# Performance work log

Measured on AMD Instinct MI355X. Metric: run time of the kernel, lower is better.

## Reference

```python
import jax, jax.numpy as jnp
import numpy as np

C = 256      # hidden_dim
H = 8        # num_head
D = 6        # depth
NQ = 100     # num_queries
B = 4        # view pairs
FEAT_HW = [64, 32, 16, 8]


def setup_inputs() -> dict:
    key = jax.random.key(0)
    ws = C ** -0.5  # weight init scale (xavier-like)
    inp = {}
    i = 0
    def nk():
        nonlocal i
        i += 1
        return jax.random.fold_in(key, i)
    for v in (1, 2):
        for l, hw in enumerate(FEAT_HW, 1):
            inp[f"feat{v}_{l}"] = jax.random.normal(nk(), (B, C, hw, hw), jnp.float32)
    inp["query_embed"] = jax.random.uniform(nk(), (NQ, C), jnp.float32)
    inp["ca_ng"] = jnp.ones((D, C), jnp.float32)
    inp["ca_nb"] = jnp.zeros((D, C), jnp.float32)
    inp["ca_wq"] = jax.random.normal(nk(), (D, C, C), jnp.float32) * ws
    inp["ca_wk"] = jax.random.normal(nk(), (D, C, C), jnp.float32) * ws
    inp["ca_wv"] = jax.random.normal(nk(), (D, C, C), jnp.float32) * ws
    inp["ca_wp"] = jax.random.normal(nk(), (D, C, C), jnp.float32) * ws
    inp["ca_bp"] = jnp.zeros((D, C), jnp.float32)
    inp["sa_wqkv"] = jax.random.normal(nk(), (D, C, 3 * C), jnp.float32) * ws
    inp["sa_wp"] = jax.random.normal(nk(), (D, C, C), jnp.float32) * ws
    inp["sa_bp"] = jnp.zeros((D, C), jnp.float32)
    return inp


def _ln(x, g, b):
    m = jnp.mean(x, axis=-1, keepdims=True)
    v = jnp.mean((x - m) ** 2, axis=-1, keepdims=True)
    return (x - m) * jax.lax.rsqrt(v + 1e-5) * g + b


def _mha(q, k, v):
    # q: [B,Nq,C], k,v: [B,Nk,C] -> [B,Nq,C]
    b, nq, _ = q.shape
    nk = k.shape[1]
    hd = C // H
    q = q.reshape(b, nq, H, hd)
    k = k.reshape(b, nk, H, hd)
    v = v.reshape(b, nk, H, hd)
    a = jnp.einsum('bqhd,bkhd->bhqk', q, k) * (hd ** -0.5)
    a = jax.nn.softmax(a, axis=-1)
    o = jnp.einsum('bhqk,bkhd->bqhd', a, v)
    return o.reshape(b, nq, C)


def reference(feat1_1, feat1_2, feat1_3, feat1_4,
              feat2_1, feat2_2, feat2_3, feat2_4,
              query_embed, ca_ng, ca_nb, ca_wq, ca_wk, ca_wv, ca_wp, ca_bp,
              sa_wqkv, sa_wp, sa_bp):
    def tok(f):  # [B,C,h,w] -> [B,h*w,C]
        return f.reshape(f.shape[0], C, -1).transpose(0, 2, 1)
    feats1 = [tok(f) for f in (feat1_1, feat1_2, feat1_3, feat1_4)]
    feats2 = [tok(f) for f in (feat2_1, feat2_2, feat2_3, feat2_4)]
    outs = []
    for f1, f2 in zip(feats1, feats2):
        q = jnp.broadcast_to(query_embed, (B, NQ, C))
        for d in range(D):
            # self attention (output replaces queries, as in the source)
            qkv = q @ sa_wqkv[d]
            qq, kk, vv = jnp.split(qkv, 3, axis=-1)
            q = _mha(qq, kk, vv) @ sa_wp[d] + sa_bp[d]
            # cross attention into each view's feature tokens
            def cross(xq, xkv):
                qn = _ln(xq, ca_ng[d], ca_nb[d]) @ ca_wq[d]
                kn = _ln(xkv, ca_ng[d], ca_nb[d]) @ ca_wk[d]
                vn = _ln(xkv, ca_ng[d], ca_nb[d]) @ ca_wv[d]
                return _mha(qn, kn, vn) @ ca_wp[d] + ca_bp[d]
            q1 = cross(q, f1)
            q2 = cross(q, f2)
            ms = jnp.einsum('bic,bjc->bij', q1, q2)  # [B,NQ,NQ] matching score
            r1 = q1 + jnp.einsum('bij,bjd->bid', jax.nn.softmax(ms, axis=2), q2)
            r2 = q2 + jnp.einsum('bij,bid->bjd', jax.nn.softmax(ms, axis=1), q1)
            q = jax.nn.softmax(q + r1 + r2, axis=-1)
        outs.append(q)
    return jnp.stack(outs)  # [num_layers, B, NQ, C]
```

## Files before the change

### kernel.cpp

```cpp
#include <hip/hip_runtime.h>


#define DI __device__ __forceinline__
#define MFMA16(a, b, c) __builtin_amdgcn_mfma_f32_16x16x32_bf16(a, b, c, 0, 0, 0)

typedef __attribute__((ext_vector_type(8))) short bf16x8;
typedef __attribute__((ext_vector_type(8))) unsigned short u16x8;
typedef __attribute__((ext_vector_type(4))) float f32x4;

constexpr long KVV = 5570560;

constexpr long O_KH    = 0;
constexpr long O_KL    = O_KH    + 5570560;
constexpr long O_VTH   = O_KL    + 5570560;
constexpr long O_VTL   = O_VTH   + 5570560;
constexpr long O_QBUF  = O_VTL   + 5570560;
constexpr long O_QKV   = O_QBUF  + 409600;
constexpr long O_QSA   = O_QKV   + 1228800;
constexpr long O_QHAT  = O_QSA   + 409600;
constexpr long O_QN    = O_QHAT  + 409600;
constexpr long O_SAO   = O_QN    + 409600;
constexpr long O_OCA   = O_SAO   + 409600;
constexpr long O_Q12   = O_OCA   + 819200;
constexpr long O_QH    = O_Q12   + 819200;
constexpr long O_QL    = O_QH    + 208896;
constexpr long O_WTH   = O_QL    + 208896;
constexpr long O_WTL   = O_WTH   + 393216;
constexpr long O_WQH   = O_WTL   + 393216;
constexpr long O_WQL   = O_WQH   + 196608;
constexpr long O_BKV   = O_WQL   + 196608;
constexpr long O_BQ    = O_BKV   + 3072;
constexpr long O_PO    = O_BQ    + 1536;
constexpr long O_PM    = O_PO    + 409600;
constexpr long O_PL    = O_PM    + 16384;
constexpr long O_PO2   = O_PL    + 16384;
constexpr long O_PM2   = O_PO2   + 3145728;
constexpr long O_PL2   = O_PM2   + 98304;
constexpr long O_MS    = O_PL2   + 98304;
constexpr long O_RST   = O_MS    + 262144;
constexpr long O_STATS = O_RST   + 8192;
constexpr long O_XH    = O_STATS + 87040;
constexpr long O_XL    = O_XH    + 5570560;
constexpr long O_SQKVH = O_XL    + 5570560;
constexpr long O_SQKVL = O_SQKVH + 589824;
constexpr long O_SWPH  = O_SQKVL + 589824;
constexpr long O_SWPL  = O_SWPH  + 196608;
constexpr long O_WPH   = O_SWPL  + 196608;
constexpr long O_WPL   = O_WPH   + 196608;
constexpr long WS_FLOATS = O_WPL + 196608;

DI int sel4(int4 v, int i) { return i == 0 ? v.x : (i == 1 ? v.y : (i == 2 ? v.z : v.w)); }
DI float dot4(float4 a, float4 b) {
  float s = a.x * b.x;
  s = fmaf(a.y, b.y, s); s = fmaf(a.z, b.z, s); s = fmaf(a.w, b.w, s);
  return s;
}
DI unsigned short bf_rne(float x) {
  unsigned u = __float_as_uint(x);
  u += 0x7fffu + ((u >> 16) & 1u);
  return (unsigned short)(u >> 16);
}
DI float bf2f(unsigned short h) { return __uint_as_float(((unsigned)h) << 16); }
DI long frag_off(int nblk_base, int k, int n) {
  return ((long)(nblk_base + (n >> 4)) * 8 + (k >> 5)) * 512 +
         ((((k & 31) >> 3)) * 16 + (n & 15)) * 8 + (k & 7);
}

__global__ void fold_w2_kernel(const float* __restrict__ ng, const float* __restrict__ wk,
                               const float* __restrict__ wv, const float* __restrict__ wq,
                               unsigned short* __restrict__ WTh, unsigned short* __restrict__ WTl,
                               unsigned short* __restrict__ WQh, unsigned short* __restrict__ WQl) {
  long idx = (long)blockIdx.x * 256 + threadIdx.x;
  const long T1 = 6L * 512 * 256;
  if (idx < T1) {
    int d = idx / (512 * 256); int r = idx % (512 * 256); int n = r / 256; int k = r % 256;
    float g = ng[d * 256 + k];
    float w = (n < 256) ? wk[((long)(d * 256 + k)) * 256 + n]
                        : wv[((long)(d * 256 + k)) * 256 + (n - 256)];
    w *= g;
    unsigned short hi = bf_rne(w);
    long off = frag_off(d * 32, k, n);
    WTh[off] = hi;
    WTl[off] = bf_rne(w - bf2f(hi));
  } else {
    long j = idx - T1;
    if (j < 6L * 256 * 256) {
      int d = j / 65536; int r = j % 65536; int k = r / 256; int n = r % 256;
      float w = ng[d * 256 + k] * wq[((long)(d * 256 + k)) * 256 + n];
      unsigned short hi = bf_rne(w);
      long off = frag_off(d * 16, k, n);
      WQh[off] = hi;
      WQl[off] = bf_rne(w - bf2f(hi));
    }
  }
}

__global__ void split_wall_kernel(const float* __restrict__ swqkv,
                                  const float* __restrict__ swp,
                                  const float* __restrict__ wp,
                                  unsigned short* __restrict__ SQh, unsigned short* __restrict__ SQl,
                                  unsigned short* __restrict__ SPh, unsigned short* __restrict__ SPl,
                                  unsigned short* __restrict__ WPh, unsigned short* __restrict__ WPl) {
  long idx = (long)blockIdx.x * 256 + threadIdx.x;
  const long T1 = 6L * 256 * 768;
  const long T2 = T1 + 6L * 256 * 256;
  const long T3 = T2 + 6L * 256 * 256;
  if (idx < T1) {
    int d = idx / 196608; int r = idx % 196608; int k = r / 768; int n = r % 768;
    float w = swqkv[idx];
    unsigned short hi = bf_rne(w);
    long off = frag_off(d * 48, k, n);
    SQh[off] = hi;
    SQl[off] = bf_rne(w - bf2f(hi));
  } else if (idx < T2) {
    long j = idx - T1;
    int d = j / 65536; int r = j % 65536; int k = r / 256; int n = r % 256;
    float w = swp[j];
    unsigned short hi = bf_rne(w);
    long off = frag_off(d * 16, k, n);
    SPh[off] = hi;
    SPl[off] = bf_rne(w - bf2f(hi));
  } else if (idx < T3) {
    long j = idx - T2;
    int d = j / 65536; int r = j % 65536; int k = r / 256; int n = r % 256;
    float w = wp[j];
    unsigned short hi = bf_rne(w);
    long off = frag_off(d * 16, k, n);
    WPh[off] = hi;
    WPl[off] = bf_rne(w - bf2f(hi));
  }
}

__global__ void fold_b_kernel(const float* __restrict__ nb, const float* __restrict__ wk,
                              const float* __restrict__ wv, const float* __restrict__ wq,
                              float* __restrict__ bkvo, float* __restrict__ bqo) {
  int idx = blockIdx.x * 256 + threadIdx.x;
  if (idx >= 6 * 768) return;
  int d = idx / 768, j = idx % 768;
  float s = 0.f;
  if (j < 256) {
    for (int c = 0; c < 256; ++c) s = fmaf(nb[d * 256 + c], wk[(d * 256 + c) * 256 + j], s);
    bkvo[d * 512 + j] = s;
  } else if (j < 512) {
    int n = j - 256;
    for (int c = 0; c < 256; ++c) s = fmaf(nb[d * 256 + c], wv[(d * 256 + c) * 256 + n], s);
    bkvo[d * 512 + j] = s;
  } else {
    int n = j - 512;
    for (int c = 0; c < 256; ++c) s = fmaf(nb[d * 256 + c], wq[(d * 256 + c) * 256 + n], s);
    bqo[d * 256 + n] = s;
  }
}

__global__ __launch_bounds__(256) void ln_stats_kernel(const float* __restrict__ feat,
                                                       float* __restrict__ stats,
                                                       int rowBase, int HW) {
  __shared__ float sred[4][64];
  __shared__ float qred[4][64];
  int b = blockIdx.y, t0 = blockIdx.x * 64;
  int tx = threadIdx.x & 63, ty = threadIdx.x >> 6;
  const float* fb = feat + (long)b * 256 * HW;
  float s = 0.f, q = 0.f;
  for (int k = 0; k < 64; ++k) {
    int c = ty * 64 + k;
    float v = fb[(long)c * HW + t0 + tx];
    s += v; q += v * v;
  }
  sred[ty][tx] = s; qred[ty][tx] = q;
  __syncthreads();
  if (ty == 0) {
    float ts = sred[0][tx] + sred[1][tx] + sred[2][tx] + sred[3][tx];
    float tq = qred[0][tx] + qred[1][tx] + qred[2][tx] + qred[3][tx];
    float m = ts * (1.f / 256.f);
    float var = tq * (1.f / 256.f) - m * m;
    int row = rowBase + b * HW + t0 + tx;
    stats[row * 2 + 0] = m;
    stats[row * 2 + 1] = rsqrtf(var + 1e-5f);
  }
}

__global__ __launch_bounds__(256) void ln_split_x_kernel(
    const float* __restrict__ f0, const float* __restrict__ f1,
    const float* __restrict__ f2, const float* __restrict__ f3,
    const float* __restrict__ stats, int vbase,
    unsigned short* __restrict__ Xh, unsigned short* __restrict__ Xl) {
  __shared__ unsigned short Th[64][66], Tl[64][66];
  int m0 = blockIdx.x * 64;
  const float* fp; int HW, rel;
  if (m0 < 16384)      { fp = f0; HW = 4096; rel = m0; }
  else if (m0 < 20480) { fp = f1; HW = 1024; rel = m0 - 16384; }
  else if (m0 < 21504) { fp = f2; HW = 256;  rel = m0 - 20480; }
  else                 { fp = f3; HW = 64;   rel = m0 - 21504; }
  int b = rel / HW, t0 = rel % HW;
  const float* fb = fp + (long)b * 256 * HW + t0;
  int t = threadIdx.x & 63, cg4 = threadIdx.x >> 6;
  float mean = stats[(vbase + m0 + t) * 2 + 0];
  float rstd = stats[(vbase + m0 + t) * 2 + 1];
  long mtb = (long)((vbase + m0) >> 4);
  int lmt = threadIdx.x >> 6, lane = threadIdx.x & 63;
  int fr = lane & 15, g = lane >> 4;
  for (int cgo = 0; cgo < 4; ++cgo) {
    if (cgo) __syncthreads();
#pragma unroll
    for (int i = 0; i < 16; ++i) {
      int c = cgo * 64 + cg4 * 16 + i;
      float x = (fb[(long)c * HW + t] - mean) * rstd;
      unsigned short hi = bf_rne(x);
      Th[t][cg4 * 16 + i] = hi;
      Tl[t][cg4 * 16 + i] = bf_rne(x - bf2f(hi));
    }
    __syncthreads();
#pragma unroll
    for (int sk = 0; sk < 2; ++sk) {
      u16x8 vh = *(const u16x8*)&Th[lmt * 16 + fr][sk * 32 + 8 * g];
      u16x8 vl = *(const u16x8*)&Tl[lmt * 16 + fr][sk * 32 + 8 * g];
      long dst = ((mtb + lmt) * 8 + cgo * 2 + sk) * 512 + lane * 8;
      *(u16x8*)&Xh[dst] = vh;
      *(u16x8*)&Xl[dst] = vl;
    }
  }
}

__global__ void init_q_kernel(const float* __restrict__ qe, float* __restrict__ qb) {
  int idx = blockIdx.x * 256 + threadIdx.x;
  if (idx < 1600 * 256) {
    int row = idx >> 8, c = idx & 255;
    qb[idx] = qe[(row % 100) * 256 + c];
  }
}

__global__ void split_q_kernel(const float* __restrict__ qn,
                               unsigned short* __restrict__ Qh,
                               unsigned short* __restrict__ Ql) {
  int idx = blockIdx.x * 256 + threadIdx.x;
  if (idx >= 1632 * 256) return;
  float v = (idx < 1600 * 256) ? qn[idx] * 0.17677669529663689f : 0.f;
  unsigned short hi = bf_rne(v);
  Qh[idx] = hi;
  Ql[idx] = bf_rne(v - bf2f(hi));
}

__global__ __launch_bounds__(256) void gemm_mfma_kernel(
    const float* __restrict__ A,
    const unsigned short* __restrict__ Wh, const unsigned short* __restrict__ Wl,
    const float* __restrict__ bias, float* __restrict__ C, int N) {
  __shared__ unsigned short Ah[2][8][512], Al[2][8][512];
  int n0 = blockIdx.x * 128;
  int m0 = blockIdx.y * 32;
  int tid = threadIdx.x;
  int w = tid >> 6, lane = tid & 63;
  int fr = lane & 15, g = lane >> 4;
#pragma unroll
  for (int mt = 0; mt < 2; ++mt)
#pragma unroll
    for (int kk = 0; kk < 2; ++kk) {
      int ks = 2 * w + kk;
      const float* src = &A[(long)(m0 + mt * 16 + fr) * 256 + ks * 32 + 8 * g];
      float4 f0 = *(const float4*)src;
      float4 f1 = *(const float4*)(src + 4);
      float vals[8] = {f0.x, f0.y, f0.z, f0.w, f1.x, f1.y, f1.z, f1.w};
      union { u16x8 v; unsigned short us[8]; } hh, ll;
#pragma unroll
      for (int e = 0; e < 8; ++e) {
        unsigned short hi = bf_rne(vals[e]);
        hh.us[e] = hi;
        ll.us[e] = bf_rne(vals[e] - bf2f(hi));
      }
      *(u16x8*)&Ah[mt][ks][lane * 8] = hh.v;
      *(u16x8*)&Al[mt][ks][lane * 8] = ll.v;
    }
  __syncthreads();
  f32x4 acc[2][2];
#pragma unroll
  for (int c4 = 0; c4 < 2; ++c4)
#pragma unroll
    for (int mt = 0; mt < 2; ++mt)
#pragma unroll
      for (int r = 0; r < 4; ++r) acc[c4][mt][r] = 0.f;
  for (int ks = 0; ks < 8; ++ks) {
    bf16x8 ah[2], al[2], wh[2], wl[2];
#pragma unroll
    for (int mt = 0; mt < 2; ++mt) {
      ah[mt] = *(const bf16x8*)&Ah[mt][ks][lane * 8];
      al[mt] = *(const bf16x8*)&Al[mt][ks][lane * 8];
    }
#pragma unroll
    for (int c4 = 0; c4 < 2; ++c4) {
      long wb = ((long)((n0 >> 4) + w * 2 + c4) * 8 + ks) * 512 + lane * 8;
      wh[c4] = *(const bf16x8*)&Wh[wb];
      wl[c4] = *(const bf16x8*)&Wl[wb];
    }
#pragma unroll
    for (int c4 = 0; c4 < 2; ++c4)
#pragma unroll
      for (int mt = 0; mt < 2; ++mt) {
        acc[c4][mt] = MFMA16(wh[c4], ah[mt], acc[c4][mt]);
        acc[c4][mt] = MFMA16(wh[c4], al[mt], acc[c4][mt]);
        acc[c4][mt] = MFMA16(wl[c4], ah[mt], acc[c4][mt]);
      }
  }
#pragma unroll
  for (int c4 = 0; c4 < 2; ++c4) {
    int nb = n0 + w * 32 + c4 * 16 + 4 * g;
    float4 bv = make_float4(0.f, 0.f, 0.f, 0.f);
    if (bias) bv = *(const float4*)&bias[nb];
#pragma unroll
    for (int mt = 0; mt < 2; ++mt) {
      int token = m0 + mt * 16 + fr;
      float4 o;
      o.x = acc[c4][mt][0] + bv.x;
      o.y = acc[c4][mt][1] + bv.y;
      o.z = acc[c4][mt][2] + bv.z;
      o.w = acc[c4][mt][3] + bv.w;
      *(float4*)&C[(long)token * N + nb] = o;
    }
  }
}

__global__ __launch_bounds__(256) void gemm_kv8_kernel(
    const unsigned short* __restrict__ Xh, const unsigned short* __restrict__ Xl,
    const unsigned short* __restrict__ Wh, const unsigned short* __restrict__ Wl,
    const float* __restrict__ bias,
    unsigned short* __restrict__ Kh, unsigned short* __restrict__ Kl,
    unsigned short* __restrict__ VTh, unsigned short* __restrict__ VTl) {
  __shared__ unsigned short Tls[18432];
  int nh = blockIdx.x;
  int m0 = blockIdx.y * 64;
  int v = blockIdx.z;
  int tid = threadIdx.x;
  int w = tid >> 6, lane = tid & 63;
  int fr = lane & 15, g = lane >> 4;
  long xmtb = (long)(v * 1360 + blockIdx.y * 4);
  f32x4 acc[4][4];
#pragma unroll
  for (int c4 = 0; c4 < 4; ++c4)
#pragma unroll
    for (int mt = 0; mt < 4; ++mt)
#pragma unroll
      for (int r = 0; r < 4; ++r) acc[c4][mt][r] = 0.f;
  for (int ks = 0; ks < 8; ++ks) {
    bf16x8 xh_[4], xl_[4], wh_[4], wl_[4];
#pragma unroll
    for (int mt = 0; mt < 4; ++mt) {
      long ar = ((xmtb + mt) * 8 + ks) * 512 + lane * 8;
      xh_[mt] = *(const bf16x8*)&Xh[ar];
      xl_[mt] = *(const bf16x8*)&Xl[ar];
    }
#pragma unroll
    for (int c4 = 0; c4 < 4; ++c4) {
      long br = ((long)(nh * 16 + c4 * 4 + w) * 8 + ks) * 512 + lane * 8;
      wh_[c4] = *(const bf16x8*)&Wh[br];
      wl_[c4] = *(const bf16x8*)&Wl[br];
    }
    if (nh == 0) {
#pragma unroll
      for (int c4 = 0; c4 < 4; ++c4)
#pragma unroll
        for (int mt = 0; mt < 4; ++mt) {
          acc[c4][mt] = MFMA16(wh_[c4], xh_[mt], acc[c4][mt]);
          acc[c4][mt] = MFMA16(wh_[c4], xl_[mt], acc[c4][mt]);
          acc[c4][mt] = MFMA16(wl_[c4], xh_[mt], acc[c4][mt]);
        }
    } else {
#pragma unroll
      for (int c4 = 0; c4 < 4; ++c4)
#pragma unroll
        for (int mt = 0; mt < 4; ++mt) {
          acc[c4][mt] = MFMA16(xh_[mt], wh_[c4], acc[c4][mt]);
          acc[c4][mt] = MFMA16(xl_[mt], wh_[c4], acc[c4][mt]);
          acc[c4][mt] = MFMA16(xh_[mt], wl_[c4], acc[c4][mt]);
        }
    }
  }
  long kvoff = (long)v * KVV;
  long tbb = (long)(m0 >> 5);
  if (nh == 0) {
    for (int part = 0; part < 2; ++part) {
      __syncthreads();
#pragma unroll
      for (int c4 = 0; c4 < 4; ++c4) {
        int nb = c4 * 64 + w * 16 + 4 * g;
        float4 bv4 = *(const float4*)&bias[nb];
        float bvs[4] = {bv4.x, bv4.y, bv4.z, bv4.w};
#pragma unroll
        for (int mt = 0; mt < 4; ++mt) {
          int tok = mt * 16 + fr;
          ushort4 u;
#pragma unroll
          for (int r = 0; r < 4; ++r) {
            float val = acc[c4][mt][r] + bvs[r];
            unsigned short hi = bf_rne(val);
            ((unsigned short*)&u)[r] = (part == 0) ? hi : bf_rne(val - bf2f(hi));
          }
          *(ushort4*)&Tls[tok * 264 + nb] = u;
        }
      }
      __syncthreads();
      unsigned short* dst = (part == 0) ? Kh : Kl;
#pragma unroll
      for (int i = 0; i < 8; ++i) {
        int gid = tid + 256 * i;
        int lane2 = gid & 63;
        int rest = gid >> 6;
        int t16 = rest & 1;
        int h2 = (rest >> 1) & 7;
        int tb_loc = rest >> 4;
        int fr2 = lane2 & 15, g2 = lane2 >> 4;
        int row = tb_loc * 32 + 8 * (fr2 >> 2) + (fr2 & 3) + 4 * t16;
        u16x8 val = *(const u16x8*)&Tls[row * 264 + h2 * 32 + 8 * g2];
        long off = kvoff + (((tbb + tb_loc) * 8 + h2) * 2 + t16) * 512 + lane2 * 8;
        *(u16x8*)&dst[off] = val;
      }
    }
  } else {
    for (int part = 0; part < 2; ++part) {
      __syncthreads();
#pragma unroll
      for (int c4 = 0; c4 < 4; ++c4) {
        int nv = c4 * 64 + w * 16 + fr;
        float bv = bias[256 + nv];
#pragma unroll
        for (int mt = 0; mt < 4; ++mt) {
          int tok = mt * 16 + 4 * g;
          ushort4 u;
#pragma unroll
          for (int r = 0; r < 4; ++r) {
            float val = acc[c4][mt][r] + bv;
            unsigned short hi = bf_rne(val);
            ((unsigned short*)&u)[r] = (part == 0) ? hi : bf_rne(val - bf2f(hi));
          }
          *(ushort4*)&Tls[nv * 72 + tok] = u;
        }
      }
      __syncthreads();
      unsigned short* dst = (part == 0) ? VTh : VTl;
#pragma unroll
      for (int i = 0; i < 8; ++i) {
        int gid = tid + 256 * i;
        int lane2 = gid & 63;
        int rest = gid >> 6;
        int d16 = rest & 1;
        int h2 = (rest >> 1) & 7;
        int tb_loc = rest >> 4;
        int fr2 = lane2 & 15, g2 = lane2 >> 4;
        int row = h2 * 32 + d16 * 16 + fr2;
        int col = tb_loc * 32 + 8 * g2;
        u16x8 val = *(const u16x8*)&Tls[row * 72 + col];
        long off = kvoff + (((tbb + tb_loc) * 8 + h2) * 2 + d16) * 512 + lane2 * 8;
        *(u16x8*)&dst[off] = val;
      }
    }
  }
}

__global__ __launch_bounds__(256) void row_ln_kernel(const float* __restrict__ in,
                                                     float* __restrict__ out) {
  __shared__ float s1[4], s2[4];
  long r = blockIdx.x;
  float x = in[r * 256 + threadIdx.x];
  float vs = x, vq = x * x;
  for (int o = 32; o; o >>= 1) { vs += __shfl_xor(vs, o); vq += __shfl_xor(vq, o); }
  int w = threadIdx.x >> 6;
  if ((threadIdx.x & 63) == 0) { s1[w] = vs; s2[w] = vq; }
  __syncthreads();
  float ts = s1[0] + s1[1] + s1[2] + s1[3];
  float tq = s2[0] + s2[1] + s2[2] + s2[3];
  float m = ts * (1.f / 256.f);
  float var = tq * (1.f / 256.f) - m * m;
  out[r * 256 + threadIdx.x] = (x - m) * rsqrtf(var + 1e-5f);
}

__global__ __launch_bounds__(256) void flash_kernel(const float* __restrict__ qp, int qld,
                                                    const float* __restrict__ kb,
                                                    const float* __restrict__ vb, int kvld,
                                                    int4 startv, int4 nchv, int4 nkv,
                                                    int4 koffv, int4 kstrbv,
                                                    float* __restrict__ po,
                                                    float* __restrict__ pm,
                                                    float* __restrict__ pl) {
  __shared__ float Kt[32][36];
  __shared__ float Vt[32][36];
  int bid = blockIdx.x;
  int s1 = startv.y, s2 = startv.z, s3 = startv.w;
  int l = (bid < s1) ? 0 : (bid < s2) ? 1 : (bid < s3) ? 2 : 3;
  int r = bid - sel4(startv, l);
  int nc = sel4(nchv, l);
  int b = r / (8 * nc);
  int h = (r / nc) & 7;
  int ch = r % nc;
  int Nk = sel4(nkv, l);
  int qr0 = (l * 4 + b) * 100;
  int kr0 = sel4(koffv, l) + b * sel4(kstrbv, l);
  int j0 = ch * 128;
  int jn = min(128, Nk - j0);
  int tiles = (jn + 31) >> 5;
  int tid = threadIdx.x;
  int qi = tid >> 1, half = tid & 1, ho = half * 16, jb = half * 16;
  const float SC = 0.17677669529663689f;
  float4 q8[8];
  if (qi < 100) {
    const float* qrow = qp + (long)(qr0 + qi) * qld + h * 32;
#pragma unroll
    for (int k = 0; k < 8; ++k) {
      float4 f = *(const float4*)&qrow[4 * k];
      q8[k] = make_float4(f.x * SC, f.y * SC, f.z * SC, f.w * SC);
    }
  } else {
#pragma unroll
    for (int k = 0; k < 8; ++k) q8[k] = make_float4(0.f, 0.f, 0.f, 0.f);
  }
  float m = -1e30f, lsum = 0.f;
  float o[16];
#pragma unroll
  for (int i = 0; i < 16; ++i) o[i] = 0.f;

  for (int kt = 0; kt < tiles; ++kt) {
    __syncthreads();
    {
      int rr = tid >> 3, c4 = (tid & 7) * 4;
      int jr = kt * 32 + rr;
      float4 kf = make_float4(0.f, 0.f, 0.f, 0.f), vf = kf;
      if (jr < jn) {
        long g = (long)(kr0 + j0 + jr) * kvld + h * 32 + c4;
        kf = *(const float4*)&kb[g];
        vf = *(const float4*)&vb[g];
      }
      *(float4*)&Kt[rr][c4 ^ (rr & 16)] = kf;
      *(float4*)&Vt[rr][c4] = vf;
    }
    __syncthreads();
    float sv[16];
#pragma unroll
    for (int j = 0; j < 16; ++j) {
      float s = 0.f;
#pragma unroll
      for (int k4 = 0; k4 < 8; ++k4) {
        float4 kv = *(const float4*)&Kt[jb + j][(4 * k4) ^ jb];
        s = fmaf(q8[k4].x, kv.x, s); s = fmaf(q8[k4].y, kv.y, s);
        s = fmaf(q8[k4].z, kv.z, s); s = fmaf(q8[k4].w, kv.w, s);
      }
      int jglob = j0 + kt * 32 + jb + j;
      sv[j] = (jglob < Nk) ? s : -1e30f;
    }
    float tmax = sv[0];
#pragma unroll
    for (int j = 1; j < 16; ++j) tmax = fmaxf(tmax, sv[j]);
    tmax = fmaxf(tmax, __shfl_xor(tmax, 1));
    float mnew = fmaxf(m, tmax);
    float scale = __expf(m - mnew);
    float p[16]; float psum = 0.f;
#pragma unroll
    for (int j = 0; j < 16; ++j) {
      int jglob = j0 + kt * 32 + jb + j;
      float e = (jglob < Nk) ? __expf(sv[j] - mnew) : 0.f;
      p[j] = e; psum += e;
    }
    psum += __shfl_xor(psum, 1);
    lsum = lsum * scale + psum;
    m = mnew;
#pragma unroll
    for (int i = 0; i < 16; ++i) o[i] *= scale;
    float pO[16];
#pragma unroll
    for (int j = 0; j < 16; ++j) pO[j] = __shfl_xor(p[j], 1);
    int jbO = jb ^ 16;
#pragma unroll
    for (int j = 0; j < 16; ++j) {
      float pj = p[j];
      const float* vrow = &Vt[jb + j][ho];
#pragma unroll
      for (int k = 0; k < 4; ++k) {
        float4 v4 = *(const float4*)&vrow[4 * k];
        o[4 * k + 0] = fmaf(pj, v4.x, o[4 * k + 0]);
        o[4 * k + 1] = fmaf(pj, v4.y, o[4 * k + 1]);
        o[4 * k + 2] = fmaf(pj, v4.z, o[4 * k + 2]);
        o[4 * k + 3] = fmaf(pj, v4.w, o[4 * k + 3]);
      }
    }
#pragma unroll
    for (int j = 0; j < 16; ++j) {
      float pj = pO[j];
      const float* vrow = &Vt[jbO + j][ho];
#pragma unroll
      for (int k = 0; k < 4; ++k) {
        float4 v4 = *(const float4*)&vrow[4 * k];
        o[4 * k + 0] = fmaf(pj, v4.x, o[4 * k + 0]);
        o[4 * k + 1] = fmaf(pj, v4.y, o[4 * k + 1]);
        o[4 * k + 2] = fmaf(pj, v4.z, o[4 * k + 2]);
        o[4 * k + 3] = fmaf(pj, v4.w, o[4 * k + 3]);
      }
    }
  }
  if (qi < 100) {
    float* pod = po + (long)bid * 3200 + qi * 32 + ho;
#pragma unroll
    for (int k = 0; k < 4; ++k)
      *(float4*)&pod[4 * k] = make_float4(o[4 * k], o[4 * k + 1], o[4 * k + 2], o[4 * k + 3]);
    if (half == 0) { pm[bid * 128 + qi] = m; pl[bid * 128 + qi] = lsum; }
  }
}

__global__ __launch_bounds__(256) void combine_kernel(const float* __restrict__ po,
                                                      const float* __restrict__ pm,
                                                      const float* __restrict__ pl,
                                                      int4 startv, int4 nchv,
                                                      float* __restrict__ outp, int outld) {
  int bid = blockIdx.x;
  int l = bid >> 5, rr = bid & 31, b = rr >> 3, h = rr & 7;
  int nc = sel4(nchv, l);
  int sb = sel4(startv, l) + (b * 8 + h) * nc;
  int qr0 = (l * 4 + b) * 100;
  int idx = blockIdx.y * 256 + threadIdx.x;
  if (idx >= 3200) return;
  int qi = idx >> 5, hd = idx & 31;
  float mstar = -1e30f;
  for (int c = 0; c < nc; ++c) mstar = fmaxf(mstar, pm[(sb + c) * 128 + qi]);
  float Lt = 0.f, val = 0.f;
  for (int c = 0; c < nc; ++c) {
    float w = __expf(pm[(sb + c) * 128 + qi] - mstar);
    Lt = fmaf(w, pl[(sb + c) * 128 + qi], Lt);
    val = fmaf(w, po[(long)(sb + c) * 3200 + qi * 32 + hd], val);
  }
  outp[(long)(qr0 + qi) * outld + h * 32 + hd] = val / Lt;
}

__global__ __launch_bounds__(256) void flash_ca2_kernel(
    const unsigned short* __restrict__ Qh, const unsigned short* __restrict__ Ql,
    const unsigned short* __restrict__ Kh, const unsigned short* __restrict__ Kl,
    const unsigned short* __restrict__ VTh, const unsigned short* __restrict__ VTl,
    float* __restrict__ po, float* __restrict__ pm, float* __restrict__ pl) {
  int tid = threadIdx.x;
  int uu = blockIdx.x * 4 + (tid >> 6);
  int v = uu / 1536;
  int u = uu - v * 1536;
  int lane = tid & 63;
  int fr = lane & 15, g = lane >> 4;
  int base, lognc, koff, kstr, ntile, l;
  if (u < 1024)      { base = 0;    lognc = 3; koff = 0;     kstr = 4096; ntile = 16; l = 0; }
  else if (u < 1280) { base = 1024; lognc = 1; koff = 16384; kstr = 1024; ntile = 16; l = 1; }
  else if (u < 1408) { base = 1280; lognc = 0; koff = 20480; kstr = 256;  ntile = 8;  l = 2; }
  else               { base = 1408; lognc = 0; koff = 21504; kstr = 64;   ntile = 2;  l = 3; }
  int r = u - base;
  int qg = r & 3; r >>= 2;
  int ch = r & ((1 << lognc) - 1); r >>= lognc;
  int h = r & 7, b = r >> 3;
  long kvoff = (long)v * KVV;
  long qoff = ((long)((l * 4 + b) * 100 + qg * 32)) * 256 + h * 32 + 8 * g;
  bf16x8 qh0 = *(const bf16x8*)&Qh[qoff + fr * 256];
  bf16x8 qh1 = *(const bf16x8*)&Qh[qoff + (16 + fr) * 256];
  bf16x8 ql0 = *(const bf16x8*)&Ql[qoff + fr * 256];
  bf16x8 ql1 = *(const bf16x8*)&Ql[qoff + (16 + fr) * 256];
  int tb0 = (koff + b * kstr + ch * 512) >> 5;
  f32x4 o00 = {0.f, 0.f, 0.f, 0.f}, o01 = o00, o10 = o00, o11 = o00;
  float m0r = -1e30f, m1r = -1e30f, l0r = 0.f, l1r = 0.f;

  for (int kt = 0; kt < ntile; ++kt) {
    long fb = kvoff + (((long)(tb0 + kt) * 8 + h) * 2) * 512 + lane * 8;
    bf16x8 kh0 = *(const bf16x8*)&Kh[fb];
    bf16x8 kl0 = *(const bf16x8*)&Kl[fb];
    bf16x8 kh1 = *(const bf16x8*)&Kh[fb + 512];
    bf16x8 kl1 = *(const bf16x8*)&Kl[fb + 512];
    bf16x8 vh0 = *(const bf16x8*)&VTh[fb];
    bf16x8 vl0 = *(const bf16x8*)&VTl[fb];
    bf16x8 vh1 = *(const bf16x8*)&VTh[fb + 512];
    bf16x8 vl1 = *(const bf16x8*)&VTl[fb + 512];
    f32x4 zz = {0.f, 0.f, 0.f, 0.f};
    f32x4 s00 = zz, s01 = zz, s10 = zz, s11 = zz;
    s00 = MFMA16(kh0, qh0, s00); s00 = MFMA16(kl0, qh0, s00); s00 = MFMA16(kh0, ql0, s00);
    s01 = MFMA16(kh1, qh0, s01); s01 = MFMA16(kl1, qh0, s01); s01 = MFMA16(kh1, ql0, s01);
    s10 = MFMA16(kh0, qh1, s10); s10 = MFMA16(kl0, qh1, s10); s10 = MFMA16(kh0, ql1, s10);
    s11 = MFMA16(kh1, qh1, s11); s11 = MFMA16(kl1, qh1, s11); s11 = MFMA16(kh1, ql1, s11);
    {
      float t0 = fmaxf(fmaxf(s00[0], s00[1]), fmaxf(s00[2], s00[3]));
      float t1 = fmaxf(fmaxf(s01[0], s01[1]), fmaxf(s01[2], s01[3]));
      float tm = fmaxf(t0, t1);
      tm = fmaxf(tm, __shfl_xor(tm, 16));
      tm = fmaxf(tm, __shfl_xor(tm, 32));
      float mn = fmaxf(m0r, tm);
      float sc = __expf(m0r - mn); m0r = mn;
      float p[8]; float ps = 0.f;
#pragma unroll
      for (int i = 0; i < 4; ++i) { p[i] = __expf(s00[i] - mn); ps += p[i]; }
#pragma unroll
      for (int i = 0; i < 4; ++i) { p[4 + i] = __expf(s01[i] - mn); ps += p[4 + i]; }
      l0r = l0r * sc + ps;
      union { bf16x8 v; unsigned short us[8]; } ph, plo;
#pragma unroll
      for (int e = 0; e < 8; ++e) {
        unsigned short hi = bf_rne(p[e]);
        ph.us[e] = hi;
        plo.us[e] = bf_rne(p[e] - bf2f(hi));
      }
#pragma unroll
      for (int i = 0; i < 4; ++i) { o00[i] *= sc; o01[i] *= sc; }
      o00 = MFMA16(vh0, ph.v, o00); o00 = MFMA16(vl0, ph.v, o00); o00 = MFMA16(vh0, plo.v, o00);
      o01 = MFMA16(vh1, ph.v, o01); o01 = MFMA16(vl1, ph.v, o01); o01 = MFMA16(vh1, plo.v, o01);
    }
    {
      float t0 = fmaxf(fmaxf(s10[0], s10[1]), fmaxf(s10[2], s10[3]));
      float t1 = fmaxf(fmaxf(s11[0], s11[1]), fmaxf(s11[2], s11[3]));
      float tm = fmaxf(t0, t1);
      tm = fmaxf(tm, __shfl_xor(tm, 16));
      tm = fmaxf(tm, __shfl_xor(tm, 32));
      float mn = fmaxf(m1r, tm);
      float sc = __expf(m1r - mn); m1r = mn;
      float p[8]; float ps = 0.f;
#pragma unroll
      for (int i = 0; i < 4; ++i) { p[i] = __expf(s10[i] - mn); ps += p[i]; }
#pragma unroll
      for (int i = 0; i < 4; ++i) { p[4 + i] = __expf(s11[i] - mn); ps += p[4 + i]; }
      l1r = l1r * sc + ps;
      union { bf16x8 v; unsigned short us[8]; } ph, plo;
#pragma unroll
      for (int e = 0; e < 8; ++e) {
        unsigned short hi = bf_rne(p[e]);
        ph.us[e] = hi;
        plo.us[e] = bf_rne(p[e] - bf2f(hi));
      }
#pragma unroll
      for (int i = 0; i < 4; ++i) { o10[i] *= sc; o11[i] *= sc; }
      o10 = MFMA16(vh0, ph.v, o10); o10 = MFMA16(vl0, ph.v, o10); o10 = MFMA16(vh0, plo.v, o10);
      o11 = MFMA16(vh1, ph.v, o11); o11 = MFMA16(vl1, ph.v, o11); o11 = MFMA16(vh1, plo.v, o11);
    }
  }
  l0r += __shfl_xor(l0r, 16); l0r += __shfl_xor(l0r, 32);
  l1r += __shfl_xor(l1r, 16); l1r += __shfl_xor(l1r, 32);
  long pob = (long)uu * 1024;
  *(f32x4*)&po[pob + fr * 32 + 4 * g] = o00;
  *(f32x4*)&po[pob + fr * 32 + 16 + 4 * g] = o01;
  *(f32x4*)&po[pob + (16 + fr) * 32 + 4 * g] = o10;
  *(f32x4*)&po[pob + (16 + fr) * 32 + 16 + 4 * g] = o11;
  if (g == 0) {
    pm[uu * 32 + fr] = m0r;       pl[uu * 32 + fr] = l0r;
    pm[uu * 32 + 16 + fr] = m1r;  pl[uu * 32 + 16 + fr] = l1r;
  }
}

__global__ __launch_bounds__(256) void combine2_kernel(const float* __restrict__ po,
                                                       const float* __restrict__ pm,
                                                       const float* __restrict__ pl,
                                                       float* __restrict__ oca) {
  int gu = blockIdx.x;
  int v = gu >> 9;
  int u = gu & 511;
  int l = u >> 7, ur = u & 127;
  int b = ur >> 5, h = (ur >> 2) & 7, qg = ur & 3;
  int nc, base;
  if (l == 0)      { nc = 8; base = 0; }
  else if (l == 1) { nc = 2; base = 1024; }
  else if (l == 2) { nc = 1; base = 1280; }
  else             { nc = 1; base = 1408; }
  int pu0 = v * 1536 + base + ((b * 8 + h) * nc) * 4 + qg;
  int qr0 = (l * 4 + b) * 100 + qg * 32;
  int qn = min(32, 100 - qg * 32);
  float* outp = oca + (long)v * 409600;
  for (int e = threadIdx.x; e < 1024; e += 256) {
    int qi = e >> 5, d = e & 31;
    if (qi >= qn) continue;
    float mstar = -1e30f;
    for (int c = 0; c < nc; ++c) mstar = fmaxf(mstar, pm[(pu0 + 4 * c) * 32 + qi]);
    float Lt = 0.f, val = 0.f;
    for (int c = 0; c < nc; ++c) {
      float w = __expf(pm[(pu0 + 4 * c) * 32 + qi] - mstar);
      Lt = fmaf(w, pl[(pu0 + 4 * c) * 32 + qi], Lt);
      val = fmaf(w, po[(long)(pu0 + 4 * c) * 1024 + qi * 32 + d], val);
    }
    outp[(long)(qr0 + qi) * 256 + h * 32 + d] = val / Lt;
  }
}

__global__ __launch_bounds__(256) void fuse_ms_kernel(const float* __restrict__ q1,
                                                      const float* __restrict__ q2,
                                                      float* __restrict__ ms) {
  __shared__ float a[32][132];
  __shared__ float bsh[32][132];
  int lb = blockIdx.x;
  int it = blockIdx.y >> 2, jt = blockIdx.y & 3;
  int tid = threadIdx.x;
  int ti = tid & 15, tj = tid >> 4;
  float acc[2][2] = {};
  for (int chalf = 0; chalf < 2; ++chalf) {
    __syncthreads();
#pragma unroll
    for (int k = 0; k < 4; ++k) {
      int i = tid + k * 256;
      int rr = i >> 5, c4 = (i & 31) * 4;
      int row1 = it * 32 + rr, row2 = jt * 32 + rr;
      float4 fa = make_float4(0.f, 0.f, 0.f, 0.f), fb = fa;
      if (row1 < 100) fa = *(const float4*)&q1[(long)(lb * 100 + row1) * 256 + chalf * 128 + c4];
      if (row2 < 100) fb = *(const float4*)&q2[(long)(lb * 100 + row2) * 256 + chalf * 128 + c4];
      *(float4*)&a[rr][c4] = fa;
      *(float4*)&bsh[rr][c4] = fb;
    }
    __syncthreads();
#pragma unroll
    for (int k4 = 0; k4 < 32; ++k4) {
      float4 a0 = *(const float4*)&a[2 * ti][4 * k4];
      float4 a1 = *(const float4*)&a[2 * ti + 1][4 * k4];
      float4 b0 = *(const float4*)&bsh[2 * tj][4 * k4];
      float4 b1 = *(const float4*)&bsh[2 * tj + 1][4 * k4];
      acc[0][0] += dot4(a0, b0); acc[0][1] += dot4(a0, b1);
      acc[1][0] += dot4(a1, b0); acc[1][1] += dot4(a1, b1);
    }
  }
#pragma unroll
  for (int i = 0; i < 2; ++i)
#pragma unroll
    for (int j = 0; j < 2; ++j)
      ms[(long)(lb * 128 + it * 32 + 2 * ti + i) * 128 + jt * 32 + 2 * tj + j] = acc[i][j];
}

__global__ void fuse_stats_kernel(const float* __restrict__ ms, float* __restrict__ rst) {
  int lb = blockIdx.x, tid = threadIdx.x;
  if (tid < 100) {
    const float* row = ms + (long)(lb * 128 + tid) * 128;
    float mx = row[0];
    for (int j = 1; j < 100; ++j) mx = fmaxf(mx, row[j]);
    float s = 0.f;
    for (int j = 0; j < 100; ++j) s += __expf(row[j] - mx);
    rst[(0 * 16 + lb) * 128 + tid] = mx;
    rst[(1 * 16 + lb) * 128 + tid] = s;
  } else if (tid >= 128 && tid < 228) {
    int j = tid - 128;
    const float* colp = ms + (long)lb * 128 * 128 + j;
    float mx = colp[0];
    for (int i = 1; i < 100; ++i) mx = fmaxf(mx, colp[i * 128]);
    float s = 0.f;
    for (int i = 0; i < 100; ++i) s += __expf(colp[i * 128] - mx);
    rst[(2 * 16 + lb) * 128 + j] = mx;
    rst[(3 * 16 + lb) * 128 + j] = s;
  }
}

__global__ __launch_bounds__(256) void fuse_apply_kernel(const float* __restrict__ ms,
                                                         const float* __restrict__ rst,
                                                         const float* __restrict__ q1,
                                                         const float* __restrict__ q2,
                                                         const float* __restrict__ qsa,
                                                         float* __restrict__ qout) {
  __shared__ float pr[100], pc[100];
  __shared__ float red1[4], red2[4];
  int lb = blockIdx.x, i = blockIdx.y, tid = threadIdx.x;
  long r = lb * 100 + i;
  if (tid < 100) {
    float rm = rst[(0 * 16 + lb) * 128 + i], rs = rst[(1 * 16 + lb) * 128 + i];
    pr[tid] = __expf(ms[(long)(lb * 128 + i) * 128 + tid] - rm) / rs;
  } else if (tid >= 128 && tid < 228) {
    int i2 = tid - 128;
    float cm = rst[(2 * 16 + lb) * 128 + i], cs = rst[(3 * 16 + lb) * 128 + i];
    pc[i2] = __expf(ms[(long)(lb * 128 + i2) * 128 + i] - cm) / cs;
  }
  __syncthreads();
  float acc1 = 0.f, acc2 = 0.f;
  for (int j = 0; j < 100; ++j) acc1 = fmaf(pr[j], q2[(long)(lb * 100 + j) * 256 + tid], acc1);
  for (int j = 0; j < 100; ++j) acc2 = fmaf(pc[j], q1[(long)(lb * 100 + j) * 256 + tid], acc2);
  float z = qsa[r * 256 + tid] + q1[r * 256 + tid] + acc1 + q2[r * 256 + tid] + acc2;
  float v = z;
  for (int off = 32; off; off >>= 1) v = fmaxf(v, __shfl_xor(v, off));
  int w = tid >> 6;
  if ((tid & 63) == 0) red1[w] = v;
  __syncthreads();
  float zm = fmaxf(fmaxf(red1[0], red1[1]), fmaxf(red1[2], red1[3]));
  float e = __expf(z - zm);
  float sv = e;
  for (int off = 32; off; off >>= 1) sv += __shfl_xor(sv, off);
  if ((tid & 63) == 0) red2[w] = sv;
  __syncthreads();
  float es = red2[0] + red2[1] + red2[2] + red2[3];
  qout[r * 256 + tid] = e / es;
}

extern "C" void kernel_launch(void* const* d_in, const int* in_sizes, int n_in,
                              void* d_out, int out_size, void* d_ws, size_t ws_size,
                              hipStream_t stream) {
  (void)in_sizes; (void)n_in; (void)out_size; (void)ws_size;
  const float* feats[2][4] = {
      {(const float*)d_in[0], (const float*)d_in[1], (const float*)d_in[2], (const float*)d_in[3]},
      {(const float*)d_in[4], (const float*)d_in[5], (const float*)d_in[6], (const float*)d_in[7]}};
  const float* qe   = (const float*)d_in[8];
  const float* ng   = (const float*)d_in[9];
  const float* nb   = (const float*)d_in[10];
  const float* wq   = (const float*)d_in[11];
  const float* wk   = (const float*)d_in[12];
  const float* wv   = (const float*)d_in[13];
  const float* wp   = (const float*)d_in[14];
  const float* bp   = (const float*)d_in[15];
  const float* swqkv= (const float*)d_in[16];
  const float* swp  = (const float*)d_in[17];
  const float* sbp  = (const float*)d_in[18];

  float* ws = (float*)d_ws;
  unsigned short* KHp  = (unsigned short*)(ws + O_KH);
  unsigned short* KLp  = (unsigned short*)(ws + O_KL);
  unsigned short* VTHp = (unsigned short*)(ws + O_VTH);
  unsigned short* VTLp = (unsigned short*)(ws + O_VTL);
  float* QBUFp = ws + O_QBUF;
  float* QKVp  = ws + O_QKV;
  float* QSAp  = ws + O_QSA;
  float* QHATp = ws + O_QHAT;
  float* QNp   = ws + O_QN;
  float* SAOp  = ws + O_SAO;
  float* OCAp  = ws + O_OCA;
  float* Q12p  = ws + O_Q12;
  unsigned short* QHp  = (unsigned short*)(ws + O_QH);
  unsigned short* QLp  = (unsigned short*)(ws + O_QL);
  unsigned short* WTHp = (unsigned short*)(ws + O_WTH);
  unsigned short* WTLp = (unsigned short*)(ws + O_WTL);
  unsigned short* WQHp = (unsigned short*)(ws + O_WQH);
  unsigned short* WQLp = (unsigned short*)(ws + O_WQL);
  float* BKVp  = ws + O_BKV;
  float* BQp   = ws + O_BQ;
  float* POp   = ws + O_PO;
  float* PMp   = ws + O_PM;
  float* PLp   = ws + O_PL;
  float* PO2p  = ws + O_PO2;
  float* PM2p  = ws + O_PM2;
  float* PL2p  = ws + O_PL2;
  float* MSp   = ws + O_MS;
  float* RSTp  = ws + O_RST;
  float* STATSp= ws + O_STATS;
  unsigned short* XHp  = (unsigned short*)(ws + O_XH);
  unsigned short* XLp  = (unsigned short*)(ws + O_XL);
  unsigned short* SQHp = (unsigned short*)(ws + O_SQKVH);
  unsigned short* SQLp = (unsigned short*)(ws + O_SQKVL);
  unsigned short* SPHp = (unsigned short*)(ws + O_SWPH);
  unsigned short* SPLp = (unsigned short*)(ws + O_SWPL);
  unsigned short* WPHp = (unsigned short*)(ws + O_WPH);
  unsigned short* WPLp = (unsigned short*)(ws + O_WPL);

  const int HWs[4] = {4096, 1024, 256, 64};
  const int VOs[4] = {0, 16384, 20480, 21504};

  fold_w2_kernel<<<4608, 256, 0, stream>>>(ng, wk, wv, wq, WTHp, WTLp, WQHp, WQLp);
  split_wall_kernel<<<7680, 256, 0, stream>>>(swqkv, swp, wp, SQHp, SQLp, SPHp, SPLp, WPHp, WPLp);
  fold_b_kernel<<<18, 256, 0, stream>>>(nb, wk, wv, wq, BKVp, BQp);
  for (int v = 0; v < 2; ++v)
    for (int l = 0; l < 4; ++l)
      ln_stats_kernel<<<dim3(HWs[l] / 64, 4), 256, 0, stream>>>(
          feats[v][l], STATSp, v * 21760 + VOs[l], HWs[l]);
  for (int v = 0; v < 2; ++v)
    ln_split_x_kernel<<<340, 256, 0, stream>>>(
        feats[v][0], feats[v][1], feats[v][2], feats[v][3], STATSp, v * 21760, XHp, XLp);
  init_q_kernel<<<1600, 256, 0, stream>>>(qe, QBUFp);

  const int4 saStart = make_int4(0, 32, 64, 96);
  const int4 saNch   = make_int4(1, 1, 1, 1);
  const int4 saNk    = make_int4(100, 100, 100, 100);
  const int4 saKoff  = make_int4(0, 400, 800, 1200);
  const int4 saKstrb = make_int4(100, 100, 100, 100);

  for (int d = 0; d < 6; ++d) {
    gemm_mfma_kernel<<<dim3(6, 50), 256, 0, stream>>>(
        QBUFp, SQHp + (long)d * 196608, SQLp + (long)d * 196608, nullptr, QKVp, 768);
    flash_kernel<<<128, 256, 0, stream>>>(QKVp, 768, QKVp + 256, QKVp + 512, 768,
                                          saStart, saNch, saNk, saKoff, saKstrb, POp, PMp, PLp);
    combine_kernel<<<dim3(128, 13), 256, 0, stream>>>(POp, PMp, PLp, saStart, saNch, SAOp, 256);
    gemm_mfma_kernel<<<dim3(2, 50), 256, 0, stream>>>(
        SAOp, SPHp + (long)d * 65536, SPLp + (long)d * 65536, sbp + d * 256, QSAp, 256);
    row_ln_kernel<<<1600, 256, 0, stream>>>(QSAp, QHATp);
    gemm_mfma_kernel<<<dim3(2, 50), 256, 0, stream>>>(
        QHATp, WQHp + (long)d * 65536, WQLp + (long)d * 65536, BQp + d * 256, QNp, 256);
    split_q_kernel<<<1632, 256, 0, stream>>>(QNp, QHp, QLp);
    gemm_kv8_kernel<<<dim3(2, 340, 2), 256, 0, stream>>>(
        XHp, XLp, WTHp + (long)d * 131072, WTLp + (long)d * 131072, BKVp + d * 512,
        KHp, KLp, VTHp, VTLp);
    flash_ca2_kernel<<<768, 256, 0, stream>>>(QHp, QLp, KHp, KLp, VTHp, VTLp,
                                              PO2p, PM2p, PL2p);
    combine2_kernel<<<1024, 256, 0, stream>>>(PO2p, PM2p, PL2p, OCAp);
    gemm_mfma_kernel<<<dim3(2, 100), 256, 0, stream>>>(
        OCAp, WPHp + (long)d * 65536, WPLp + (long)d * 65536, bp + d * 256, Q12p, 256);
    fuse_ms_kernel<<<dim3(16, 16), 256, 0, stream>>>(Q12p, Q12p + 409600, MSp);
    fuse_stats_kernel<<<16, 256, 0, stream>>>(MSp, RSTp);
    fuse_apply_kernel<<<dim3(16, 100), 256, 0, stream>>>(MSp, RSTp, Q12p, Q12p + 409600,
                                                         QSAp, QBUFp);
  }
  hipMemcpyAsync(d_out, QBUFp, 409600 * sizeof(float), hipMemcpyDeviceToDevice, stream);
}
```

Baseline: 1.373 ms.

## Fuse Q split into GEMM epilogue, inline softmax stats, remap KV grid

```diff
diff --git a/kernel.cpp b/kernel.cpp
--- a/kernel.cpp
+++ b/kernel.cpp
@@ -50,11 +50,6 @@
 constexpr long WS_FLOATS = O_WPL + 196608;
 
 DI int sel4(int4 v, int i) { return i == 0 ? v.x : (i == 1 ? v.y : (i == 2 ? v.z : v.w)); }
-DI float dot4(float4 a, float4 b) {
-  float s = a.x * b.x;
-  s = fmaf(a.y, b.y, s); s = fmaf(a.z, b.z, s); s = fmaf(a.w, b.w, s);
-  return s;
-}
 DI unsigned short bf_rne(float x) {
   unsigned u = __float_as_uint(x);
   u += 0x7fffu + ((u >> 16) & 1u);
@@ -152,6 +147,15 @@
   }
 }
 
+__global__ void zero_qpad_kernel(unsigned short* __restrict__ Qh,
+                                 unsigned short* __restrict__ Ql) {
+  int idx = blockIdx.x * 256 + threadIdx.x;
+  if (idx < 32 * 256) {
+    Qh[1600 * 256 + idx] = 0;
+    Ql[1600 * 256 + idx] = 0;
+  }
+}
+
 __global__ __launch_bounds__(256) void ln_stats_kernel(const float* __restrict__ feat,
                                                        float* __restrict__ stats,
                                                        int rowBase, int HW) {
@@ -229,17 +233,6 @@
   }
 }
 
-__global__ void split_q_kernel(const float* __restrict__ qn,
-                               unsigned short* __restrict__ Qh,
-                               unsigned short* __restrict__ Ql) {
-  int idx = blockIdx.x * 256 + threadIdx.x;
-  if (idx >= 1632 * 256) return;
-  float v = (idx < 1600 * 256) ? qn[idx] * 0.17677669529663689f : 0.f;
-  unsigned short hi = bf_rne(v);
-  Qh[idx] = hi;
-  Ql[idx] = bf_rne(v - bf2f(hi));
-}
-
 __global__ __launch_bounds__(256) void gemm_mfma_kernel(
     const float* __restrict__ A,
     const unsigned short* __restrict__ Wh, const unsigned short* __restrict__ Wl,
@@ -317,6 +310,89 @@
   }
 }
 
+__global__ __launch_bounds__(256) void gemm_mfma_q_kernel(
+    const float* __restrict__ A,
+    const unsigned short* __restrict__ Wh, const unsigned short* __restrict__ Wl,
+    const float* __restrict__ bias,
+    unsigned short* __restrict__ Qh, unsigned short* __restrict__ Ql) {
+  __shared__ unsigned short Ah[2][8][512], Al[2][8][512];
+  int n0 = blockIdx.x * 128;
+  int m0 = blockIdx.y * 32;
+  int tid = threadIdx.x;
+  int w = tid >> 6, lane = tid & 63;
+  int fr = lane & 15, g = lane >> 4;
+  const float SC = 0.17677669529663689f;
+#pragma unroll
+  for (int mt = 0; mt < 2; ++mt)
+#pragma unroll
+    for (int kk = 0; kk < 2; ++kk) {
+      int ks = 2 * w + kk;
+      const float* src = &A[(long)(m0 + mt * 16 + fr) * 256 + ks * 32 + 8 * g];
+      float4 f0 = *(const float4*)src;
+      float4 f1 = *(const float4*)(src + 4);
+      float vals[8] = {f0.x, f0.y, f0.z, f0.w, f1.x, f1.y, f1.z, f1.w};
+      union { u16x8 v; unsigned short us[8]; } hh, ll;
+#pragma unroll
+      for (int e = 0; e < 8; ++e) {
+        unsigned short hi = bf_rne(vals[e]);
+        hh.us[e] = hi;
+        ll.us[e] = bf_rne(vals[e] - bf2f(hi));
+      }
+      *(u16x8*)&Ah[mt][ks][lane * 8] = hh.v;
+      *(u16x8*)&Al[mt][ks][lane * 8] = ll.v;
+    }
+  __syncthreads();
+  f32x4 acc[2][2];
+#pragma unroll
+  for (int c4 = 0; c4 < 2; ++c4)
+#pragma unroll
+    for (int mt = 0; mt < 2; ++mt)
+#pragma unroll
+      for (int r = 0; r < 4; ++r) acc[c4][mt][r] = 0.f;
+  for (int ks = 0; ks < 8; ++ks) {
+    bf16x8 ah[2], al[2], wh[2], wl[2];
+#pragma unroll
+    for (int mt = 0; mt < 2; ++mt) {
+      ah[mt] = *(const bf16x8*)&Ah[mt][ks][lane * 8];
+      al[mt] = *(const bf16x8*)&Al[mt][ks][lane * 8];
+    }
+#pragma unroll
+    for (int c4 = 0; c4 < 2; ++c4) {
+      long wb = ((long)((n0 >> 4) + w * 2 + c4) * 8 + ks) * 512 + lane * 8;
+      wh[c4] = *(const bf16x8*)&Wh[wb];
+      wl[c4] = *(const bf16x8*)&Wl[wb];
+    }
+#pragma unroll
+    for (int c4 = 0; c4 < 2; ++c4)
+#pragma unroll
+      for (int mt = 0; mt < 2; ++mt) {
+        acc[c4][mt] = MFMA16(wh[c4], ah[mt], acc[c4][mt]);
+        acc[c4][mt] = MFMA16(wh[c4], al[mt], acc[c4][mt]);
+        acc[c4][mt] = MFMA16(wl[c4], ah[mt], acc[c4][mt]);
+      }
+  }
+#pragma unroll
+  for (int c4 = 0; c4 < 2; ++c4) {
+    int nb = n0 + w * 32 + c4 * 16 + 4 * g;
+    float4 bv = *(const float4*)&bias[nb];
+    float bvs[4] = {bv.x, bv.y, bv.z, bv.w};
+#pragma unroll
+    for (int mt = 0; mt < 2; ++mt) {
+      int token = m0 + mt * 16 + fr;
+      ushort4 uh, ul;
+#pragma unroll
+      for (int r = 0; r < 4; ++r) {
+        float val = (acc[c4][mt][r] + bvs[r]) * SC;
+        unsigned short hi = bf_rne(val);
+        ((unsigned short*)&uh)[r] = hi;
+        ((unsigned short*)&ul)[r] = bf_rne(val - bf2f(hi));
+      }
+      *(ushort4*)&Qh[(long)token * 256 + nb] = uh;
+      *(ushort4*)&Ql[(long)token * 256 + nb] = ul;
+    }
+  }
+}
+
 __global__ __launch_bounds__(256) void gemm_kv8_kernel(
     const unsigned short* __restrict__ Xh, const unsigned short* __restrict__ Xl,
     const unsigned short* __restrict__ Wh, const unsigned short* __restrict__ Wl,
@@ -324,13 +400,16 @@
     unsigned short* __restrict__ Kh, unsigned short* __restrict__ Kl,
     unsigned short* __restrict__ VTh, unsigned short* __restrict__ VTl) {
   __shared__ unsigned short Tls[18432];
-  int nh = blockIdx.x;
-  int m0 = blockIdx.y * 64;
-  int v = blockIdx.z;
+  int bid = blockIdx.x;
+  int nh = (bid >> 3) & 1;
+  int t = (bid & 7) | ((bid >> 4) << 3);
+  int v = t / 340;
+  int mi = t - v * 340;
+  int m0 = mi * 64;
   int tid = threadIdx.x;
   int w = tid >> 6, lane = tid & 63;
   int fr = lane & 15, g = lane >> 4;
-  long xmtb = (long)(v * 1360 + blockIdx.y * 4);
+  long xmtb = (long)(v * 1360 + mi * 4);
   f32x4 acc[4][4];
 #pragma unroll
   for (int c4 = 0; c4 < 4; ++c4)
@@ -769,6 +848,11 @@
   }
 }
 
+DI float dot4(float4 a, float4 b) {
+  float s = a.x * b.x;
+  s = fmaf(a.y, b.y, s); s = fmaf(a.z, b.z, s); s = fmaf(a.w, b.w, s);
+  return s;
+}
 __global__ __launch_bounds__(256) void fuse_ms_kernel(const float* __restrict__ q1,
                                                       const float* __restrict__ q2,
                                                       float* __restrict__ ms) {
@@ -810,50 +894,55 @@
       ms[(long)(lb * 128 + it * 32 + 2 * ti + i) * 128 + jt * 32 + 2 * tj + j] = acc[i][j];
 }
 
-__global__ void fuse_stats_kernel(const float* __restrict__ ms, float* __restrict__ rst) {
-  int lb = blockIdx.x, tid = threadIdx.x;
-  if (tid < 100) {
-    const float* row = ms + (long)(lb * 128 + tid) * 128;
-    float mx = row[0];
-    for (int j = 1; j < 100; ++j) mx = fmaxf(mx, row[j]);
-    float s = 0.f;
-    for (int j = 0; j < 100; ++j) s += __expf(row[j] - mx);
-    rst[(0 * 16 + lb) * 128 + tid] = mx;
-    rst[(1 * 16 + lb) * 128 + tid] = s;
-  } else if (tid >= 128 && tid < 228) {
-    int j = tid - 128;
-    const float* colp = ms + (long)lb * 128 * 128 + j;
-    float mx = colp[0];
-    for (int i = 1; i < 100; ++i) mx = fmaxf(mx, colp[i * 128]);
-    float s = 0.f;
-    for (int i = 0; i < 100; ++i) s += __expf(colp[i * 128] - mx);
-    rst[(2 * 16 + lb) * 128 + j] = mx;
-    rst[(3 * 16 + lb) * 128 + j] = s;
-  }
-}
-
 __global__ __launch_bounds__(256) void fuse_apply_kernel(const float* __restrict__ ms,
-                                                         const float* __restrict__ rst,
                                                          const float* __restrict__ q1,
                                                          const float* __restrict__ q2,
                                                          const float* __restrict__ qsa,
                                                          float* __restrict__ qout) {
-  __shared__ float pr[100], pc[100];
+  __shared__ float pr[128], pc[128];
+  __shared__ float red[8];
   __shared__ float red1[4], red2[4];
   int lb = blockIdx.x, i = blockIdx.y, tid = threadIdx.x;
   long r = lb * 100 + i;
-  if (tid < 100) {
-    float rm = rst[(0 * 16 + lb) * 128 + i], rs = rst[(1 * 16 + lb) * 128 + i];
-    pr[tid] = __expf(ms[(long)(lb * 128 + i) * 128 + tid] - rm) / rs;
-  } else if (tid >= 128 && tid < 228) {
-    int i2 = tid - 128;
-    float cm = rst[(2 * 16 + lb) * 128 + i], cs = rst[(3 * 16 + lb) * 128 + i];
-    pc[i2] = __expf(ms[(long)(lb * 128 + i2) * 128 + i] - cm) / cs;
-  }
+  if (tid < 128)
+    pr[tid] = (tid < 100) ? ms[(long)(lb * 128 + i) * 128 + tid] : -1e30f;
+  else
+    pc[tid - 128] = (tid < 228) ? ms[(long)(lb * 128 + (tid - 128)) * 128 + i] : -1e30f;
   __syncthreads();
+  if (tid < 64) {
+    float mx = fmaxf(pr[tid], pr[tid + 64]);
+    for (int o = 32; o; o >>= 1) mx = fmaxf(mx, __shfl_xor(mx, o));
+    if (tid == 0) red[0] = mx;
+  } else if (tid >= 128 && tid < 192) {
+    int t2 = tid - 128;
+    float mx = fmaxf(pc[t2], pc[t2 + 64]);
+    for (int o = 32; o; o >>= 1) mx = fmaxf(mx, __shfl_xor(mx, o));
+    if (t2 == 0) red[2] = mx;
+  }
+  __syncthreads();
+  float rm = red[0], cm = red[2];
+  if (tid < 128)
+    pr[tid] = (tid < 100) ? __expf(pr[tid] - rm) : 0.f;
+  else
+    pc[tid - 128] = (tid < 228) ? __expf(pc[tid - 128] - cm) : 0.f;
+  __syncthreads();
+  if (tid < 64) {
+    float sm = pr[tid] + pr[tid + 64];
+    for (int o = 32; o; o >>= 1) sm += __shfl_xor(sm, o);
+    if (tid == 0) red[1] = sm;
+  } else if (tid >= 128 && tid < 192) {
+    int t2 = tid - 128;
+    float sm = pc[t2] + pc[t2 + 64];
+    for (int o = 32; o; o >>= 1) sm += __shfl_xor(sm, o);
+    if (t2 == 0) red[3] = sm;
+  }
+  __syncthreads();
+  float rs = red[1], cs = red[3];
   float acc1 = 0.f, acc2 = 0.f;
   for (int j = 0; j < 100; ++j) acc1 = fmaf(pr[j], q2[(long)(lb * 100 + j) * 256 + tid], acc1);
   for (int j = 0; j < 100; ++j) acc2 = fmaf(pc[j], q1[(long)(lb * 100 + j) * 256 + tid], acc2);
+  acc1 /= rs;
+  acc2 /= cs;
   float z = qsa[r * 256 + tid] + q1[r * 256 + tid] + acc1 + q2[r * 256 + tid] + acc2;
   float v = z;
   for (int off = 32; off; off >>= 1) v = fmaxf(v, __shfl_xor(v, off));
@@ -898,7 +987,6 @@
   float* QKVp  = ws + O_QKV;
   float* QSAp  = ws + O_QSA;
   float* QHATp = ws + O_QHAT;
-  float* QNp   = ws + O_QN;
   float* SAOp  = ws + O_SAO;
   float* OCAp  = ws + O_OCA;
   float* Q12p  = ws + O_Q12;
@@ -917,7 +1005,6 @@
   float* PM2p  = ws + O_PM2;
   float* PL2p  = ws + O_PL2;
   float* MSp   = ws + O_MS;
-  float* RSTp  = ws + O_RST;
   float* STATSp= ws + O_STATS;
   unsigned short* XHp  = (unsigned short*)(ws + O_XH);
   unsigned short* XLp  = (unsigned short*)(ws + O_XL);
@@ -934,6 +1021,7 @@
   fold_w2_kernel<<<4608, 256, 0, stream>>>(ng, wk, wv, wq, WTHp, WTLp, WQHp, WQLp);
   split_wall_kernel<<<7680, 256, 0, stream>>>(swqkv, swp, wp, SQHp, SQLp, SPHp, SPLp, WPHp, WPLp);
   fold_b_kernel<<<18, 256, 0, stream>>>(nb, wk, wv, wq, BKVp, BQp);
+  zero_qpad_kernel<<<32, 256, 0, stream>>>(QHp, QLp);
   for (int v = 0; v < 2; ++v)
     for (int l = 0; l < 4; ++l)
       ln_stats_kernel<<<dim3(HWs[l] / 64, 4), 256, 0, stream>>>(
@@ -958,10 +1046,9 @@
     gemm_mfma_kernel<<<dim3(2, 50), 256, 0, stream>>>(
         SAOp, SPHp + (long)d * 65536, SPLp + (long)d * 65536, sbp + d * 256, QSAp, 256);
     row_ln_kernel<<<1600, 256, 0, stream>>>(QSAp, QHATp);
-    gemm_mfma_kernel<<<dim3(2, 50), 256, 0, stream>>>(
-        QHATp, WQHp + (long)d * 65536, WQLp + (long)d * 65536, BQp + d * 256, QNp, 256);
-    split_q_kernel<<<1632, 256, 0, stream>>>(QNp, QHp, QLp);
-    gemm_kv8_kernel<<<dim3(2, 340, 2), 256, 0, stream>>>(
+    gemm_mfma_q_kernel<<<dim3(2, 50), 256, 0, stream>>>(
+        QHATp, WQHp + (long)d * 65536, WQLp + (long)d * 65536, BQp + d * 256, QHp, QLp);
+    gemm_kv8_kernel<<<1360, 256, 0, stream>>>(
         XHp, XLp, WTHp + (long)d * 131072, WTLp + (long)d * 131072, BKVp + d * 512,
         KHp, KLp, VTHp, VTLp);
     flash_ca2_kernel<<<768, 256, 0, stream>>>(QHp, QLp, KHp, KLp, VTHp, VTLp,
@@ -970,8 +1057,7 @@
     gemm_mfma_kernel<<<dim3(2, 100), 256, 0, stream>>>(
         OCAp, WPHp + (long)d * 65536, WPLp + (long)d * 65536, bp + d * 256, Q12p, 256);
     fuse_ms_kernel<<<dim3(16, 16), 256, 0, stream>>>(Q12p, Q12p + 409600, MSp);
-    fuse_stats_kernel<<<16, 256, 0, stream>>>(MSp, RSTp);
-    fuse_apply_kernel<<<dim3(16, 100), 256, 0, stream>>>(MSp, RSTp, Q12p, Q12p + 409600,
+    fuse_apply_kernel<<<dim3(16, 100), 256, 0, stream>>>(MSp, Q12p, Q12p + 409600,
                                                          QSAp, QBUFp);
   }
   hipMemcpyAsync(d_out, QBUFp, 409600 * sizeof(float), hipMemcpyDeviceToDevice, stream);
```

After: 1.259 ms. 8.3% less time.
